# Performance work log

Measured on AMD Instinct MI355X. Metric: run time of the kernel, lower is better.

The kernel has to match this reference:

```python
import jax, jax.numpy as jnp
import numpy as np

N_NODES = 100000
N_EDGES = 2000000
F_IN = 64
HID = 64
N_MP = 6  # hidden message-passing layers


def setup_inputs() -> dict:
    key = jax.random.key(0)
    ks = jax.random.split(key, 8)
    x = jax.random.normal(ks[0], (N_NODES, F_IN), dtype=jnp.float32)
    edge_index = jax.random.randint(ks[1], (2, N_EDGES), 0, N_NODES, dtype=jnp.int64)
    # GCNConv params: weight [in, out], bias [out] (glorot-ish scale)
    def w(k, i, o):
        return jax.random.normal(k, (i, o), dtype=jnp.float32) * (1.0 / np.sqrt(i))
    W_i = w(ks[2], F_IN, HID)
    b_i = jnp.zeros((HID,), jnp.float32)
    W_h = jax.random.normal(ks[3], (N_MP, HID, HID), dtype=jnp.float32) * (1.0 / np.sqrt(HID))
    b_h = jnp.zeros((N_MP, HID), jnp.float32)
    W_o = w(ks[4], HID, 1)
    b_o = jnp.zeros((1,), jnp.float32)
    return {"x": x, "edge_index": edge_index, "W_i": W_i, "b_i": b_i,
            "W_h": W_h, "b_h": b_h, "W_o": W_o, "b_o": b_o}


def reference(x, edge_index, W_i, b_i, W_h, b_h, W_o, b_o):
    n = x.shape[0]
    loop = jnp.arange(n, dtype=edge_index.dtype)
    # add self loops (PyG GCNConv default)
    src = jnp.concatenate([edge_index[0], loop])  # [E+N]
    dst = jnp.concatenate([edge_index[1], loop])
    # symmetric normalization: deg computed over dst (col) with self loops
    deg = jax.ops.segment_sum(jnp.ones(dst.shape, x.dtype), dst, num_segments=n)
    dinv = jax.lax.rsqrt(deg)  # deg >= 1 due to self loops
    norm = (dinv[src] * dinv[dst])[:, None]  # [E+N, 1]

    def conv(h, W, b):
        h = h @ W                                   # [N, out]
        msg = h[src] * norm                         # gather + scale  [E+N, out]
        return jax.ops.segment_sum(msg, dst, num_segments=n) + b

    h = jax.nn.relu(conv(x, W_i, b_i))
    for l in range(W_h.shape[0]):
        h = jax.nn.relu(conv(h, W_h[l], b_h[l]))
    return conv(h, W_o, b_o)  # [N, 1]
```

## Files before the change

kernel.cpp:

```cpp
#include <hip/hip_runtime.h>
#include <math.h>

#define TPB 256
#define BSH 7
#define NPB (1 << BSH)
#define BMAX 1024
#define EPB 4096


__global__ __launch_bounds__(TPB) void k_hist(const int* __restrict__ dst,
                                              int* __restrict__ bucketCnt,
                                              int nE, int nbuck) {
  __shared__ int h[BMAX];
  for (int i = threadIdx.x; i < BMAX; i += TPB) h[i] = 0;
  __syncthreads();
  int base = blockIdx.x * EPB;
  for (int i = threadIdx.x; i < EPB; i += TPB) {
    int e = base + i;
    if (e < nE) atomicAdd(&h[dst[e] >> BSH], 1);
  }
  __syncthreads();
  for (int i = threadIdx.x; i < nbuck; i += TPB)
    if (h[i]) atomicAdd(&bucketCnt[i], h[i]);
}

__global__ __launch_bounds__(BMAX) void k_bscan(const int* __restrict__ bucketCnt,
                                                int* __restrict__ bOff,
                                                int* __restrict__ gCur,
                                                int* __restrict__ rowPtr,
                                                int nbuck, int n, int nE) {
  __shared__ int sd[BMAX];
  int t = threadIdx.x;
  int v = (t < nbuck) ? bucketCnt[t] : 0;
  sd[t] = v;
  __syncthreads();
  for (int off = 1; off < BMAX; off <<= 1) {
    int add = (t >= off) ? sd[t - off] : 0;
    __syncthreads();
    sd[t] += add;
    __syncthreads();
  }
  if (t < nbuck) {
    bOff[t + 1] = sd[t];
    gCur[t] = sd[t] - v;
  }
  if (t == 0) { bOff[0] = 0; rowPtr[n] = nE; }
}

__global__ __launch_bounds__(TPB) void k_bucket(const int* __restrict__ src,
                                                const int* __restrict__ dst,
                                                int* __restrict__ gCur,
                                                int* __restrict__ pairBuf,
                                                int nE, int nbuck) {
  __shared__ int   hist[BMAX];
  __shared__ int   baseL[BMAX];
  __shared__ int   sp[EPB];
  __shared__ short sbk[EPB];
  for (int i = threadIdx.x; i < BMAX; i += TPB) hist[i] = 0;
  __syncthreads();
  int cb = blockIdx.x * EPB;
  for (int i = threadIdx.x; i < EPB; i += TPB) {
    int e = cb + i;
    if (e < nE) {
      int s = src[e], d = dst[e];
      int b = d >> BSH;
      sp[i]  = s | ((d & (NPB - 1)) << 20);
      sbk[i] = (short)b;
      atomicAdd(&hist[b], 1);
    } else sbk[i] = -1;
  }
  __syncthreads();
  for (int i = threadIdx.x; i < nbuck; i += TPB)
    baseL[i] = hist[i] ? atomicAdd(&gCur[i], hist[i]) : 0;
  __syncthreads();
  for (int i = threadIdx.x; i < BMAX; i += TPB) hist[i] = 0;
  __syncthreads();
  for (int i = threadIdx.x; i < EPB; i += TPB) {
    int b = sbk[i];
    if (b >= 0) {
      int r = atomicAdd(&hist[b], 1);
      pairBuf[baseL[b] + r] = sp[i];
    }
  }
}

__global__ __launch_bounds__(TPB) void k_final(const int* __restrict__ pairBuf,
                                               const int* __restrict__ bOff,
                                               int* __restrict__ rowPtr,
                                               int* __restrict__ col,
                                               float* __restrict__ dinv,
                                               int n) {
  __shared__ int h[NPB];
  __shared__ int ex[NPB];
  int t = threadIdx.x;
  int b = blockIdx.x;
  int p0 = bOff[b], p1 = bOff[b + 1];
  if (t < NPB) h[t] = 0;
  __syncthreads();
  for (int i = p0 + t; i < p1; i += TPB)
    atomicAdd(&h[pairBuf[i] >> 20], 1);
  __syncthreads();
  int v = 0;
  if (t < NPB) { v = h[t]; ex[t] = v; }
  __syncthreads();
  for (int off = 1; off < NPB; off <<= 1) {
    int add = 0;
    if (t < NPB && t >= off) add = ex[t - off];
    __syncthreads();
    if (t < NPB) ex[t] += add;
    __syncthreads();
  }
  if (t < NPB) {
    int node = (b << BSH) + t;
    if (node < n) {
      int excl = ex[t] - v;
      rowPtr[node] = p0 + excl;
      dinv[node]   = rsqrtf((float)(v + 1));
      h[t] = excl;
    }
  }
  __syncthreads();
  for (int i = p0 + t; i < p1; i += TPB) {
    int p = pairBuf[i];
    int r = atomicAdd(&h[p >> 20], 1);
    col[p0 + r] = p & 0xFFFFF;
  }
}


__global__ __launch_bounds__(TPB, 4) void k_gemm(const float* __restrict__ H,
                                                 const float* __restrict__ W,
                                                 const float* __restrict__ dinv,
                                                 float* __restrict__ HWS,
                                                 int relu, int denseIn,
                                                 int rows, int N8) {
  __shared__ float Wl[64 * 64];
  __shared__ float Hl[64][68];
  const int tid = threadIdx.x;
  const int c0 = (tid & 15) * 4;
  const int r0 = (tid >> 4) * 4;
  const int row0 = blockIdx.x * 64;

  for (int i = tid; i < 64 * 16; i += TPB)
    ((float4*)Wl)[i] = ((const float4*)W)[i];

  if (denseIn) {
    for (int i = tid; i < 64 * 16; i += TPB) {
      int r = i >> 4, q = i & 15;
      int gr = row0 + r;
      float4 v = make_float4(0.f, 0.f, 0.f, 0.f);
      if (gr < rows) v = ((const float4*)(H + (size_t)gr * 64))[q];
      if (relu) {
        v.x = fmaxf(v.x, 0.f); v.y = fmaxf(v.y, 0.f);
        v.z = fmaxf(v.z, 0.f); v.w = fmaxf(v.w, 0.f);
      }
      *(float4*)&Hl[r][q * 4] = v;
    }
  } else {
    for (int i = tid; i < 64 * 16; i += TPB) {
      int s = i >> 7, j = i & 127, r = j >> 1, half = j & 1;
      int gr = row0 + r;
      float4 v = make_float4(0.f, 0.f, 0.f, 0.f);
      if (gr < rows)
        v = *(const float4*)&H[(size_t)s * N8 + (size_t)gr * 8 + half * 4];
      if (relu) {
        v.x = fmaxf(v.x, 0.f); v.y = fmaxf(v.y, 0.f);
        v.z = fmaxf(v.z, 0.f); v.w = fmaxf(v.w, 0.f);
      }
      *(float4*)&Hl[r][s * 8 + half * 4] = v;
    }
  }
  __syncthreads();

  float acc[4][4] = {{0.f,0.f,0.f,0.f},{0.f,0.f,0.f,0.f},
                     {0.f,0.f,0.f,0.f},{0.f,0.f,0.f,0.f}};
#pragma unroll 4
  for (int k = 0; k < 64; ++k) {
    float4 w = *(const float4*)&Wl[k * 64 + c0];
    float h0 = Hl[r0 + 0][k];
    float h1 = Hl[r0 + 1][k];
    float h2 = Hl[r0 + 2][k];
    float h3 = Hl[r0 + 3][k];
    acc[0][0] = fmaf(h0, w.x, acc[0][0]); acc[0][1] = fmaf(h0, w.y, acc[0][1]);
    acc[0][2] = fmaf(h0, w.z, acc[0][2]); acc[0][3] = fmaf(h0, w.w, acc[0][3]);
    acc[1][0] = fmaf(h1, w.x, acc[1][0]); acc[1][1] = fmaf(h1, w.y, acc[1][1]);
    acc[1][2] = fmaf(h1, w.z, acc[1][2]); acc[1][3] = fmaf(h1, w.w, acc[1][3]);
    acc[2][0] = fmaf(h2, w.x, acc[2][0]); acc[2][1] = fmaf(h2, w.y, acc[2][1]);
    acc[2][2] = fmaf(h2, w.z, acc[2][2]); acc[2][3] = fmaf(h2, w.w, acc[2][3]);
    acc[3][0] = fmaf(h3, w.x, acc[3][0]); acc[3][1] = fmaf(h3, w.y, acc[3][1]);
    acc[3][2] = fmaf(h3, w.z, acc[3][2]); acc[3][3] = fmaf(h3, w.w, acc[3][3]);
  }

  const int sOut = (tid & 15) >> 1;
  const int cc   = (tid & 1) * 4;
#pragma unroll
  for (int i = 0; i < 4; ++i) {
    int gr = row0 + r0 + i;
    if (gr < rows) {
      float s = dinv[gr];
      float4 o = make_float4(acc[i][0] * s, acc[i][1] * s,
                             acc[i][2] * s, acc[i][3] * s);
      *(float4*)&HWS[(size_t)sOut * N8 + (size_t)gr * 8 + cc] = o;
    }
  }
}

__global__ __launch_bounds__(TPB) void k_scat8(const float* __restrict__ HWS,
                                               const int* __restrict__ rowPtr,
                                               const int* __restrict__ col,
                                               const float* __restrict__ dinv,
                                               const float* __restrict__ bias,
                                               float* __restrict__ OUT,
                                               int n, int N8) {
  const int slice = blockIdx.x & 7;
  const int grp   = blockIdx.x >> 3;
  const int t     = threadIdx.x;
  const int node  = grp * 32 + (t >> 3);
  const int c     = t & 7;
  if (node >= n) return;

  const float* __restrict__ tab = HWS + (size_t)slice * N8;
  float acc = tab[(size_t)node * 8 + c];

  const int e1 = rowPtr[node + 1];
  int e = rowPtr[node];
  for (; e + 8 <= e1; e += 8) {
    int i0 = col[e],     i1 = col[e + 1], i2 = col[e + 2], i3 = col[e + 3];
    int i4 = col[e + 4], i5 = col[e + 5], i6 = col[e + 6], i7 = col[e + 7];
    float v0 = tab[(size_t)i0 * 8 + c];
    float v1 = tab[(size_t)i1 * 8 + c];
    float v2 = tab[(size_t)i2 * 8 + c];
    float v3 = tab[(size_t)i3 * 8 + c];
    float v4 = tab[(size_t)i4 * 8 + c];
    float v5 = tab[(size_t)i5 * 8 + c];
    float v6 = tab[(size_t)i6 * 8 + c];
    float v7 = tab[(size_t)i7 * 8 + c];
    acc += ((v0 + v1) + (v2 + v3)) + ((v4 + v5) + (v6 + v7));
  }
  for (; e + 4 <= e1; e += 4) {
    int i0 = col[e], i1 = col[e + 1], i2 = col[e + 2], i3 = col[e + 3];
    float v0 = tab[(size_t)i0 * 8 + c];
    float v1 = tab[(size_t)i1 * 8 + c];
    float v2 = tab[(size_t)i2 * 8 + c];
    float v3 = tab[(size_t)i3 * 8 + c];
    acc += (v0 + v1) + (v2 + v3);
  }
  for (; e < e1; ++e) acc += tab[(size_t)col[e] * 8 + c];

  OUT[(size_t)slice * N8 + (size_t)node * 8 + c] =
      dinv[node] * acc + bias[slice * 8 + c];
}

__global__ __launch_bounds__(TPB) void k_fdot(const float* __restrict__ H,
                                              const float* __restrict__ Wo,
                                              const float* __restrict__ dinv,
                                              float* __restrict__ hws1,
                                              int n, int N8) {
  int i = blockIdx.x * TPB + threadIdx.x;
  if (i >= n) return;
  float acc = 0.f;
#pragma unroll
  for (int s = 0; s < 8; ++s) {
    float4 a = *(const float4*)&H[(size_t)s * N8 + (size_t)i * 8];
    float4 b = *(const float4*)&H[(size_t)s * N8 + (size_t)i * 8 + 4];
    acc += fmaxf(a.x, 0.f) * Wo[s * 8 + 0];
    acc += fmaxf(a.y, 0.f) * Wo[s * 8 + 1];
    acc += fmaxf(a.z, 0.f) * Wo[s * 8 + 2];
    acc += fmaxf(a.w, 0.f) * Wo[s * 8 + 3];
    acc += fmaxf(b.x, 0.f) * Wo[s * 8 + 4];
    acc += fmaxf(b.y, 0.f) * Wo[s * 8 + 5];
    acc += fmaxf(b.z, 0.f) * Wo[s * 8 + 6];
    acc += fmaxf(b.w, 0.f) * Wo[s * 8 + 7];
  }
  hws1[i] = acc * dinv[i];
}

__global__ __launch_bounds__(TPB) void k_fscat(const float* __restrict__ hws1,
                                               const int* __restrict__ rowPtr,
                                               const int* __restrict__ col,
                                               const float* __restrict__ dinv,
                                               const float* __restrict__ bo,
                                               float* __restrict__ out, int n) {
  int i = blockIdx.x * TPB + threadIdx.x;
  if (i >= n) return;
  float a0 = hws1[i], a1 = 0.f, a2 = 0.f, a3 = 0.f;
  int e0 = rowPtr[i], e1 = rowPtr[i + 1];
  int e = e0;
  for (; e + 4 <= e1; e += 4) {
    a0 += hws1[col[e]];
    a1 += hws1[col[e + 1]];
    a2 += hws1[col[e + 2]];
    a3 += hws1[col[e + 3]];
  }
  for (; e < e1; ++e) a0 += hws1[col[e]];
  out[i] = dinv[i] * ((a0 + a1) + (a2 + a3)) + bo[0];
}


extern "C" void kernel_launch(void* const* d_in, const int* in_sizes, int n_in,
                              void* d_out, int out_size, void* d_ws, size_t ws_size,
                              hipStream_t stream) {
  const float* x   = (const float*)d_in[0];
  const int*   ei  = (const int*)d_in[1];
  const float* W_i = (const float*)d_in[2];
  const float* b_i = (const float*)d_in[3];
  const float* W_h = (const float*)d_in[4];
  const float* b_h = (const float*)d_in[5];
  const float* W_o = (const float*)d_in[6];
  const float* b_o = (const float*)d_in[7];

  const int N = in_sizes[0] / 64;
  const int E = in_sizes[1] / 2;
  const int N8 = N * 8;
  const int* srcArr = ei;
  const int* dstArr = ei + E;
  const int nbuck = (N + NPB - 1) >> BSH;

  char* w = (char*)d_ws;
  auto take = [&](size_t bytes) -> char* {
    char* p = w;
    w += (bytes + 255) & ~(size_t)255;
    return p;
  };
  int*   rowPtr    = (int*)take((size_t)(N + 1) * 4);
  int*   col       = (int*)take((size_t)E * 4);
  float* dinv      = (float*)take((size_t)N * 4);
  int*   bucketCnt = (int*)take((size_t)BMAX * 4);
  int*   bOff      = (int*)take((size_t)(BMAX + 1) * 4);
  int*   gCur      = (int*)take((size_t)BMAX * 4);
  float* bufH      = (float*)take((size_t)N * 64 * 4);
  float* bufS      = (float*)take((size_t)N * 64 * 4);
  float* hws1      = (float*)take((size_t)N * 4);
  int*   pairBuf   = (int*)bufS;
  (void)ws_size; (void)n_in; (void)out_size;

  const int nbN    = (N + TPB - 1) / TPB;
  const int nbEd   = (E + EPB - 1) / EPB;
  const int nbGemm = (N + 63) / 64;
  const int nbScat = 8 * ((N + 31) / 32);

  hipMemsetAsync(bucketCnt, 0, (size_t)BMAX * 4, stream);
  k_hist  <<<nbEd, TPB, 0, stream>>>(dstArr, bucketCnt, E, nbuck);
  k_bscan <<<1, BMAX, 0, stream>>>(bucketCnt, bOff, gCur, rowPtr, nbuck, N, E);
  k_bucket<<<nbEd, TPB, 0, stream>>>(srcArr, dstArr, gCur, pairBuf, E, nbuck);
  k_final <<<nbuck, TPB, 0, stream>>>(pairBuf, bOff, rowPtr, col, dinv, N);

  k_gemm <<<nbGemm, TPB, 0, stream>>>(x, W_i, dinv, bufS, 0, 1, N, N8);
  k_scat8<<<nbScat, TPB, 0, stream>>>(bufS, rowPtr, col, dinv, b_i, bufH, N, N8);

  for (int l = 0; l < 6; ++l) {
    k_gemm <<<nbGemm, TPB, 0, stream>>>(bufH, W_h + (size_t)l * 64 * 64, dinv, bufS, 1, 0, N, N8);
    k_scat8<<<nbScat, TPB, 0, stream>>>(bufS, rowPtr, col, dinv, b_h + (size_t)l * 64, bufH, N, N8);
  }

  k_fdot <<<nbN, TPB, 0, stream>>>(bufH, W_o, dinv, hws1, N, N8);
  k_fscat<<<nbN, TPB, 0, stream>>>(hws1, rowPtr, col, dinv, b_o, (float*)d_out, N);
}
```

Before: 879.4 us.

## Split scatter gather across edges per node with float4 loads and shuffle reduction

The CSR aggregation kernel now gives each node 16 lanes: 8 edge slots times 2 float4 halves of the 8-channel slice. Previously 8 lanes each walked the whole neighbour list loading one scalar. Each lane now reads its own subset of edges and the partial sums are combined with xor shuffles before one lane pair writes the result. This is meant to raise memory-level parallelism and cut per-node serial latency on a gather-bound kernel. In exchange it needs twice as many blocks, shuffle overhead, and idle lanes for low-degree nodes (average about 21 edges).

```diff
diff --git a/kernel.cpp b/kernel.cpp
--- a/kernel.cpp
+++ b/kernel.cpp
@@ -213,42 +213,67 @@
                                                float* __restrict__ OUT,
                                                int n, int N8) {
   const int slice = blockIdx.x & 7;
-  const int grp   = blockIdx.x >> 3;
-  const int t     = threadIdx.x;
-  const int node  = grp * 32 + (t >> 3);
-  const int c     = t & 7;
+  const int nb    = blockIdx.x >> 3;
+  const int tid   = threadIdx.x;
+  const int wv    = tid >> 6;
+  const int lane  = tid & 63;
+  const int g     = lane >> 4;
+  const int gl    = lane & 15;
+  const int es    = gl >> 1;
+  const int h     = gl & 1;
+  const int node  = nb * 16 + wv * 4 + g;
   if (node >= n) return;
 
-  const float* __restrict__ tab = HWS + (size_t)slice * N8;
-  float acc = tab[(size_t)node * 8 + c];
-
-  const int e1 = rowPtr[node + 1];
-  int e = rowPtr[node];
-  for (; e + 8 <= e1; e += 8) {
-    int i0 = col[e],     i1 = col[e + 1], i2 = col[e + 2], i3 = col[e + 3];
-    int i4 = col[e + 4], i5 = col[e + 5], i6 = col[e + 6], i7 = col[e + 7];
-    float v0 = tab[(size_t)i0 * 8 + c];
-    float v1 = tab[(size_t)i1 * 8 + c];
-    float v2 = tab[(size_t)i2 * 8 + c];
-    float v3 = tab[(size_t)i3 * 8 + c];
-    float v4 = tab[(size_t)i4 * 8 + c];
-    float v5 = tab[(size_t)i5 * 8 + c];
-    float v6 = tab[(size_t)i6 * 8 + c];
-    float v7 = tab[(size_t)i7 * 8 + c];
-    acc += ((v0 + v1) + (v2 + v3)) + ((v4 + v5) + (v6 + v7));
-  }
-  for (; e + 4 <= e1; e += 4) {
-    int i0 = col[e], i1 = col[e + 1], i2 = col[e + 2], i3 = col[e + 3];
-    float v0 = tab[(size_t)i0 * 8 + c];
-    float v1 = tab[(size_t)i1 * 8 + c];
-    float v2 = tab[(size_t)i2 * 8 + c];
-    float v3 = tab[(size_t)i3 * 8 + c];
-    acc += (v0 + v1) + (v2 + v3);
-  }
-  for (; e < e1; ++e) acc += tab[(size_t)col[e] * 8 + c];
-
-  OUT[(size_t)slice * N8 + (size_t)node * 8 + c] =
-      dinv[node] * acc + bias[slice * 8 + c];
+  const float4* __restrict__ tab = (const float4*)(HWS + (size_t)slice * N8);
+
+  float4 acc = make_float4(0.f, 0.f, 0.f, 0.f);
+  if (es == 0) acc = tab[(size_t)node * 2 + h];
+
+  const int e0  = rowPtr[node];
+  const int deg = rowPtr[node + 1] - e0;
+  const int* __restrict__ cp = col + e0;
+
+  int base = 0;
+  for (; base + 16 <= deg; base += 16) {
+    int i0 = cp[base + es];
+    int i1 = cp[base + 8 + es];
+    float4 v0 = tab[(size_t)i0 * 2 + h];
+    float4 v1 = tab[(size_t)i1 * 2 + h];
+    acc.x += v0.x + v1.x;
+    acc.y += v0.y + v1.y;
+    acc.z += v0.z + v1.z;
+    acc.w += v0.w + v1.w;
+  }
+  {
+    int j0 = base + es;
+    int j1 = base + 8 + es;
+    if (j0 < deg) {
+      int i0 = cp[j0];
+      float4 v0 = tab[(size_t)i0 * 2 + h];
+      acc.x += v0.x; acc.y += v0.y; acc.z += v0.z; acc.w += v0.w;
+    }
+    if (j1 < deg) {
+      int i1 = cp[j1];
+      float4 v1 = tab[(size_t)i1 * 2 + h];
+      acc.x += v1.x; acc.y += v1.y; acc.z += v1.z; acc.w += v1.w;
+    }
+  }
+
+#pragma unroll
+  for (int off = 2; off < 16; off <<= 1) {
+    acc.x += __shfl_xor(acc.x, off, 64);
+    acc.y += __shfl_xor(acc.y, off, 64);
+    acc.z += __shfl_xor(acc.z, off, 64);
+    acc.w += __shfl_xor(acc.w, off, 64);
+  }
+
+  if (es == 0) {
+    float s = dinv[node];
+    float4 b4 = *(const float4*)&bias[slice * 8 + h * 4];
+    float4 o = make_float4(acc.x * s + b4.x, acc.y * s + b4.y,
+                           acc.z * s + b4.z, acc.w * s + b4.w);
+    *(float4*)&OUT[(size_t)slice * N8 + (size_t)node * 8 + h * 4] = o;
+  }
 }
 
 __global__ __launch_bounds__(TPB) void k_fdot(const float* __restrict__ H,
@@ -337,7 +362,7 @@
   const int nbN    = (N + TPB - 1) / TPB;
   const int nbEd   = (E + EPB - 1) / EPB;
   const int nbGemm = (N + 63) / 64;
-  const int nbScat = 8 * ((N + 31) / 32);
+  const int nbScat = 8 * ((N + 15) / 16);
 
   hipMemsetAsync(bucketCnt, 0, (size_t)BMAX * 4, stream);
   k_hist  <<<nbEd, TPB, 0, stream>>>(dstArr, bucketCnt, E, nbuck);
```

New measurement: 870.9 us. No clear change (-1.0%).
